# Optimization experiments

Hardware: AMD Instinct MI355X
Metric: run time of the kernel (lower is better)

## Reference

```python
import jax, jax.numpy as jnp
import numpy as np

T, B, I, H, L = 2048, 64, 256, 256, 2


def setup_inputs() -> dict:
    key = jax.random.key(0)
    ks = jax.random.split(key, 11)
    s = 1.0 / np.sqrt(H)  # torch LSTMCell reset_parameters: U(-1/sqrt(H), 1/sqrt(H))
    u = lambda k, shape: jax.random.uniform(k, shape, jnp.float32, -s, s)
    return {
        "input_": jax.random.normal(ks[0], (T, B, I), jnp.float32),
        "mask": (jax.random.uniform(ks[1], (T, B)) < 0.95).astype(jnp.float32),
        "reset_indices": (jax.random.uniform(ks[2], (T, B)) < 0.02).astype(jnp.float32),
        "W_ih0": u(ks[3], (4 * H, I)),
        "W_hh0": u(ks[4], (4 * H, H)),
        "b_ih0": u(ks[5], (4 * H,)),
        "b_hh0": u(ks[6], (4 * H,)),
        "W_ih1": u(ks[7], (4 * H, H)),
        "W_hh1": u(ks[8], (4 * H, H)),
        "b_ih1": u(ks[9], (4 * H,)),
        "b_hh1": u(ks[10], (4 * H,)),
    }


def _run_layer(x, mask, reset, W_ih, W_hh, b_ih, b_hh):
    # Precompute input projection for all timesteps as one big GEMM: [T,B,4H]
    xg = jnp.einsum('tbi,gi->tbg', x, W_ih) + b_ih + b_hh
    Bx = x.shape[1]
    Hh = W_hh.shape[1]

    def step(carry, xs):
        h, c = carry
        g_x, m_t, r_t = xs
        gates = g_x + h @ W_hh.T  # [B,4H]
        i, f, g, o = jnp.split(gates, 4, axis=-1)
        c_new = jax.nn.sigmoid(f) * c + jax.nn.sigmoid(i) * jnp.tanh(g)
        h_new = jax.nn.sigmoid(o) * jnp.tanh(c_new)
        m = m_t[:, None]
        h_b = h_new * m + h * (1.0 - m)   # mask blend (variable length)
        c_b = c_new * m + c * (1.0 - m)
        r = r_t[:, None]
        return (h_b * (1.0 - r), c_b * (1.0 - r)), h_b  # reset applied AFTER output

    h0 = jnp.zeros((Bx, Hh), x.dtype)
    (h_n, c_n), out = jax.lax.scan(step, (h0, h0), (xg, mask, reset))
    return out, h_n, c_n


def reference(input_, mask, reset_indices, W_ih0, W_hh0, b_ih0, b_hh0,
              W_ih1, W_hh1, b_ih1, b_hh1):
    # Faithful quirk of the original: every layer starts from the same zero hx.
    out0, h_n0, c_n0 = _run_layer(input_, mask, reset_indices, W_ih0, W_hh0, b_ih0, b_hh0)
    out1, h_n1, c_n1 = _run_layer(out0, mask, reset_indices, W_ih1, W_hh1, b_ih1, b_hh1)
    h_n = jnp.stack([h_n0, h_n1], 0)  # [L,B,H]
    c_n = jnp.stack([c_n0, c_n1], 0)
    return out1, h_n, c_n
```

## Files before the change

kernel.cpp:

```cpp
#include <hip/hip_runtime.h>
#include <cstdint>
#include <cstddef>

#define T_STEPS 2048
#define BB 64
#define II 256
#define HH 256
#define GG 1024
#define RING 64
#define VQ 23
#define LQ 9

static_assert((RING & (RING - 1)) == 0, "RING must be power of 2");
static_assert(VQ + LQ == 32, "full K coverage");

typedef _Float16 half2_t __attribute__((ext_vector_type(2)));
typedef unsigned u32x4_t __attribute__((ext_vector_type(4)));

static __device__ __forceinline__ float sigm(float x) {
    return 1.0f / (1.0f + __expf(-x));
}
static __device__ __forceinline__ float tanhfast(float x) {
    float e = __expf(2.0f * x);
    return 1.0f - 2.0f / (e + 1.0f);
}
static __device__ __forceinline__ float fd2(unsigned hu, unsigned wu, float acc) {
    union { unsigned u; half2_t v; } a, b;
    a.u = hu; b.u = wu;
    return __builtin_amdgcn_fdot2(a.v, b.v, acc, false);
}

static __device__ __forceinline__ unsigned aloadu(const unsigned* p) {
    return __hip_atomic_load((unsigned*)p, __ATOMIC_RELAXED, __HIP_MEMORY_SCOPE_AGENT);
}
static __device__ __forceinline__ void astoreu(unsigned* p, unsigned v) {
    __hip_atomic_store(p, v, __ATOMIC_RELAXED, __HIP_MEMORY_SCOPE_AGENT);
}
static __device__ __forceinline__ int aloadi(const int* p) {
    return __hip_atomic_load((int*)p, __ATOMIC_RELAXED, __HIP_MEMORY_SCOPE_AGENT);
}
static __device__ __forceinline__ void astorei(int* p, int v) {
    __hip_atomic_store(p, v, __ATOMIC_RELAXED, __HIP_MEMORY_SCOPE_AGENT);
}
#define CFENCE asm volatile("" ::: "memory")

__global__ void k_pack_w(const float* __restrict__ W, unsigned* __restrict__ wt) {
    int p = blockIdx.x;
    int row = threadIdx.x;
    float2 v = *(const float2*)(W + (size_t)row * HH + 2 * p);
    union { unsigned u; half2_t h; } cv;
    cv.h = half2_t{ (_Float16)v.x, (_Float16)v.y };
    wt[((size_t)(p >> 2) * 1024 + row) * 4 + (p & 3)] = cv.u;
}

__global__ void k_bias_sum(const float* __restrict__ a, const float* __restrict__ b,
                           float* __restrict__ o) {
    int i = threadIdx.x;
    o[i] = a[i] + b[i];
}

__global__ void k_init_prog(int* __restrict__ p) {
    p[threadIdx.x] = 0;
}

__global__ __launch_bounds__(256, 1)
__attribute__((amdgpu_waves_per_eu(1, 1)))
void k_pipe(const float* __restrict__ x,
            const float* __restrict__ mask,
            const float* __restrict__ reset,
            const u32x4_t* __restrict__ wih0,
            const u32x4_t* __restrict__ whh0,
            const u32x4_t* __restrict__ wih1,
            const u32x4_t* __restrict__ whh1,
            const float* __restrict__ bsum0,
            const float* __restrict__ bsum1,
            unsigned* __restrict__ gx0,
            unsigned* __restrict__ gx1,
            unsigned* __restrict__ h0r,
            float* __restrict__ out,
            float* __restrict__ hn,
            float* __restrict__ cn,
            int* __restrict__ prog)
{
    __shared__ __align__(16) u32x4_t wsh[LQ * 1024];
    __shared__ __align__(16) _Float16 hbuf[2][HH];

    const int stage = blockIdx.x >> 6;
    const int b = blockIdx.x & 63;
    const int tid = threadIdx.x;
    const int r0 = tid, r1 = tid + 256, r2 = tid + 512, r3 = tid + 768;

    const u32x4_t* w4 = (stage == 0) ? wih0 : (stage == 1) ? whh0
                      : (stage == 2) ? wih1 : whh1;

#pragma unroll
    for (int j = 0; j < LQ; ++j) {
        wsh[j * 1024 + r0] = w4[(size_t)(VQ + j) * 1024 + r0];
        wsh[j * 1024 + r1] = w4[(size_t)(VQ + j) * 1024 + r1];
        wsh[j * 1024 + r2] = w4[(size_t)(VQ + j) * 1024 + r2];
        wsh[j * 1024 + r3] = w4[(size_t)(VQ + j) * 1024 + r3];
    }
    unsigned wr0[4 * VQ], wr1[4 * VQ], wr2[4 * VQ], wr3[4 * VQ];
#pragma unroll
    for (int j = 0; j < VQ; ++j) {
        u32x4_t q;
        q = w4[(size_t)j * 1024 + r0]; wr0[4*j] = q.x; wr0[4*j+1] = q.y; wr0[4*j+2] = q.z; wr0[4*j+3] = q.w;
        q = w4[(size_t)j * 1024 + r1]; wr1[4*j] = q.x; wr1[4*j+1] = q.y; wr1[4*j+2] = q.z; wr1[4*j+3] = q.w;
        q = w4[(size_t)j * 1024 + r2]; wr2[4*j] = q.x; wr2[4*j+1] = q.y; wr2[4*j+2] = q.z; wr2[4*j+3] = q.w;
        q = w4[(size_t)j * 1024 + r3]; wr3[4*j] = q.x; wr3[4*j+1] = q.y; wr3[4*j+2] = q.z; wr3[4*j+3] = q.w;
    }
#pragma unroll
    for (int j = 0; j < 4 * VQ; ++j) {
        asm volatile("" : "+v"(wr0[j]));
        asm volatile("" : "+v"(wr1[j]));
        asm volatile("" : "+v"(wr2[j]));
        asm volatile("" : "+v"(wr3[j]));
    }

    float bs0 = 0.f, bs1 = 0.f, bs2 = 0.f, bs3 = 0.f;
    if (stage == 0 || stage == 2) {
        const float* bs = (stage == 0) ? bsum0 : bsum1;
        bs0 = bs[r0]; bs1 = bs[r1]; bs2 = bs[r2]; bs3 = bs[r3];
    }
    float hp = 0.f, cp = 0.f;

    hbuf[0][tid] = (stage == 0) ? (_Float16)x[(size_t)b * II + tid] : (_Float16)0.f;
    hbuf[1][tid] = (_Float16)0.f;

    int seen = 0, bp = 0;
    int* myf = prog + stage * BB + b;
    const int* srcf = prog + (stage > 0 ? stage - 1 : 0) * BB + b;
    const int* consf = prog + (stage < 3 ? stage + 1 : 3) * BB + b;
    __syncthreads();

    for (int t = 0; t < T_STEPS; ++t) {
        float xn = 0.f, mc = 0.f, rc = 0.f;
        unsigned gA = 0, gB = 0;

        if (stage == 0) {
            if (t + 1 < T_STEPS)
                xn = x[((size_t)(t + 1) * BB + b) * II + tid];
            if (t - bp > RING - 8) {
                bp = aloadi(consf);
                while (t - bp > RING - 8) { __builtin_amdgcn_s_sleep(8); bp = aloadi(consf); }
                CFENCE;
            }
        } else if (stage == 2) {
            if (seen <= t) {
                seen = aloadi(srcf);
                while (seen <= t) { __builtin_amdgcn_s_sleep(2); seen = aloadi(srcf); }
                CFENCE;
            }
            unsigned hu = aloadu(h0r + ((size_t)(t & (RING - 1)) * BB + b) * HH + tid);
            __syncthreads();
            if (tid == 0) { astorei(myf, t); CFENCE; }
            hbuf[0][tid] = (_Float16)__uint_as_float(hu);
            if (t - bp > RING - 8) {
                bp = aloadi(consf);
                while (t - bp > RING - 8) { __builtin_amdgcn_s_sleep(8); bp = aloadi(consf); }
                CFENCE;
            }
            __syncthreads();
        } else {
            if (seen <= t) {
                seen = aloadi(srcf);
                while (seen <= t) { __builtin_amdgcn_s_sleep(2); seen = aloadi(srcf); }
                CFENCE;
            }
            const unsigned* gring = (stage == 1) ? gx0 : gx1;
            size_t gbase = ((size_t)(t & (RING - 1)) * BB + b) * 512;
            gA = aloadu(gring + gbase + tid);
            gB = aloadu(gring + gbase + 256 + tid);
            mc = mask[(size_t)t * BB + b];
            rc = reset[(size_t)t * BB + b];
            if (stage == 1 && t - bp > RING - 8) {
                bp = aloadi(consf);
                while (t - bp > RING - 8) { __builtin_amdgcn_s_sleep(8); bp = aloadi(consf); }
                CFENCE;
            }
        }

        const u32x4_t* hsh = (const u32x4_t*)((stage == 2) ? hbuf[0] : hbuf[t & 1]);
        float a00 = 0.f, a01 = 0.f, a02 = 0.f, a03 = 0.f;
        float a10 = 0.f, a11 = 0.f, a12 = 0.f, a13 = 0.f;
        float a20 = 0.f, a21 = 0.f, a22 = 0.f, a23 = 0.f;
        float a30 = 0.f, a31 = 0.f, a32 = 0.f, a33 = 0.f;
#pragma unroll
        for (int j = 0; j < VQ; ++j) {
            u32x4_t hv = hsh[j];
            a00 = fd2(hv.x, wr0[4*j+0], a00); a01 = fd2(hv.y, wr0[4*j+1], a01);
            a02 = fd2(hv.z, wr0[4*j+2], a02); a03 = fd2(hv.w, wr0[4*j+3], a03);
            a10 = fd2(hv.x, wr1[4*j+0], a10); a11 = fd2(hv.y, wr1[4*j+1], a11);
            a12 = fd2(hv.z, wr1[4*j+2], a12); a13 = fd2(hv.w, wr1[4*j+3], a13);
            a20 = fd2(hv.x, wr2[4*j+0], a20); a21 = fd2(hv.y, wr2[4*j+1], a21);
            a22 = fd2(hv.z, wr2[4*j+2], a22); a23 = fd2(hv.w, wr2[4*j+3], a23);
            a30 = fd2(hv.x, wr3[4*j+0], a30); a31 = fd2(hv.y, wr3[4*j+1], a31);
            a32 = fd2(hv.z, wr3[4*j+2], a32); a33 = fd2(hv.w, wr3[4*j+3], a33);
        }
#pragma unroll
        for (int j = 0; j < LQ; ++j) {
            u32x4_t hv = hsh[VQ + j];
            u32x4_t w0 = wsh[j * 1024 + r0];
            a00 = fd2(hv.x, w0.x, a00); a01 = fd2(hv.y, w0.y, a01);
            a02 = fd2(hv.z, w0.z, a02); a03 = fd2(hv.w, w0.w, a03);
            u32x4_t w1 = wsh[j * 1024 + r1];
            a10 = fd2(hv.x, w1.x, a10); a11 = fd2(hv.y, w1.y, a11);
            a12 = fd2(hv.z, w1.z, a12); a13 = fd2(hv.w, w1.w, a13);
            u32x4_t w2 = wsh[j * 1024 + r2];
            a20 = fd2(hv.x, w2.x, a20); a21 = fd2(hv.y, w2.y, a21);
            a22 = fd2(hv.z, w2.z, a22); a23 = fd2(hv.w, w2.w, a23);
            u32x4_t w3 = wsh[j * 1024 + r3];
            a30 = fd2(hv.x, w3.x, a30); a31 = fd2(hv.y, w3.y, a31);
            a32 = fd2(hv.z, w3.z, a32); a33 = fd2(hv.w, w3.w, a33);
        }
        float s0 = (a00 + a01) + (a02 + a03);
        float s1 = (a10 + a11) + (a12 + a13);
        float s2 = (a20 + a21) + (a22 + a23);
        float s3 = (a30 + a31) + (a32 + a33);

        if (stage == 0 || stage == 2) {
            s0 += bs0; s1 += bs1; s2 += bs2; s3 += bs3;
            unsigned* gring = (stage == 0) ? gx0 : gx1;
            size_t gbase = ((size_t)(t & (RING - 1)) * BB + b) * 512;
            union { unsigned u; half2_t h; } pa, pb;
            pa.h = half2_t{ (_Float16)s0, (_Float16)s2 };
            pb.h = half2_t{ (_Float16)s1, (_Float16)s3 };
            astoreu(gring + gbase + tid, pa.u);
            astoreu(gring + gbase + 256 + tid, pb.u);
            if (stage == 0) {
                hbuf[(t + 1) & 1][tid] = (_Float16)xn;
                __syncthreads();
                if (tid == 0) { astorei(myf, t + 1); CFENCE; }
            }
        } else {
            union { unsigned u; half2_t h; } ua, ub;
            ua.u = gA; ub.u = gB;
            float si = s0 + (float)ua.h.x;
            float sf = s1 + (float)ub.h.x;
            float sg = s2 + (float)ua.h.y;
            float so = s3 + (float)ub.h.y;
            float i_ = sigm(si), f_ = sigm(sf), g_ = tanhfast(sg), o_ = sigm(so);
            float cnew = f_ * cp + i_ * g_;
            float hnew = o_ * tanhfast(cnew);
            float hb = hnew * mc + hp * (1.f - mc);
            float cb = cnew * mc + cp * (1.f - mc);
            if (stage == 1)
                astoreu(h0r + ((size_t)(t & (RING - 1)) * BB + b) * HH + tid,
                        __float_as_uint(hb));
            else
                out[(size_t)t * (BB * HH) + (size_t)b * HH + tid] = hb;
            hp = hb * (1.f - rc);
            cp = cb * (1.f - rc);
            hbuf[(t + 1) & 1][tid] = (_Float16)hp;
            __syncthreads();
            if (tid == 0) { astorei(myf, t + 1); CFENCE; }
        }
    }

    if (stage == 2) {
        __syncthreads();
        if (tid == 0) { astorei(myf, T_STEPS); CFENCE; }
    }
    if (stage == 1 || stage == 3) {
        int L = (stage == 3);
        hn[((size_t)L * BB + b) * HH + tid] = hp;
        cn[((size_t)L * BB + b) * HH + tid] = cp;
    }
}

extern "C" void kernel_launch(void* const* d_in, const int* in_sizes, int n_in,
                              void* d_out, int out_size, void* d_ws, size_t ws_size,
                              hipStream_t stream) {
    (void)in_sizes; (void)n_in; (void)out_size; (void)ws_size;
    const float* input = (const float*)d_in[0];
    const float* maskp = (const float*)d_in[1];
    const float* resetp = (const float*)d_in[2];
    const float* Wih0 = (const float*)d_in[3];
    const float* Whh0 = (const float*)d_in[4];
    const float* bih0 = (const float*)d_in[5];
    const float* bhh0 = (const float*)d_in[6];
    const float* Wih1 = (const float*)d_in[7];
    const float* Whh1 = (const float*)d_in[8];
    const float* bih1 = (const float*)d_in[9];
    const float* bhh1 = (const float*)d_in[10];

    const size_t WPACK = (size_t)GG * HH * 2;
    char* p = (char*)d_ws;
    unsigned* wih0t = (unsigned*)p; p += WPACK;
    unsigned* whh0t = (unsigned*)p; p += WPACK;
    unsigned* wih1t = (unsigned*)p; p += WPACK;
    unsigned* whh1t = (unsigned*)p; p += WPACK;
    float* bsum0 = (float*)p; p += GG * sizeof(float);
    float* bsum1 = (float*)p; p += GG * sizeof(float);
    int* prog = (int*)p; p += 4096;
    unsigned* gx0 = (unsigned*)p; p += (size_t)RING * BB * 512 * 4;
    unsigned* gx1 = (unsigned*)p; p += (size_t)RING * BB * 512 * 4;
    unsigned* h0r = (unsigned*)p; p += (size_t)RING * BB * 256 * 4;

    float* out1 = (float*)d_out;
    float* hn = out1 + (size_t)T_STEPS * BB * HH;
    float* cn = hn + 2 * (size_t)BB * HH;

    k_pack_w<<<dim3(HH / 2), 1024, 0, stream>>>(Wih0, wih0t);
    k_pack_w<<<dim3(HH / 2), 1024, 0, stream>>>(Whh0, whh0t);
    k_pack_w<<<dim3(HH / 2), 1024, 0, stream>>>(Wih1, wih1t);
    k_pack_w<<<dim3(HH / 2), 1024, 0, stream>>>(Whh1, whh1t);
    k_bias_sum<<<dim3(1), GG, 0, stream>>>(bih0, bhh0, bsum0);
    k_bias_sum<<<dim3(1), GG, 0, stream>>>(bih1, bhh1, bsum1);
    k_init_prog<<<dim3(1), 256, 0, stream>>>(prog);

    const float* a_x = input; const float* a_m = maskp; const float* a_r = resetp;
    const u32x4_t* a_w0 = (const u32x4_t*)wih0t;
    const u32x4_t* a_w1 = (const u32x4_t*)whh0t;
    const u32x4_t* a_w2 = (const u32x4_t*)wih1t;
    const u32x4_t* a_w3 = (const u32x4_t*)whh1t;
    const float* a_b0 = bsum0; const float* a_b1 = bsum1;
    unsigned* a_g0 = gx0; unsigned* a_g1 = gx1; unsigned* a_h0 = h0r;
    float* a_out = out1; float* a_hn = hn; float* a_cn = cn; int* a_pr = prog;
    void* args[] = { &a_x, &a_m, &a_r, &a_w0, &a_w1, &a_w2, &a_w3, &a_b0, &a_b1,
                     &a_g0, &a_g1, &a_h0, &a_out, &a_hn, &a_cn, &a_pr };

    hipError_t err = hipLaunchCooperativeKernel((const void*)k_pipe, dim3(4 * BB),
                                                dim3(256), args, 0, stream);
    if (err != hipSuccess) {
        (void)hipGetLastError();
        k_pipe<<<dim3(4 * BB), dim3(256), 0, stream>>>(
            a_x, a_m, a_r, a_w0, a_w1, a_w2, a_w3, a_b0, a_b1,
            a_g0, a_g1, a_h0, a_out, a_hn, a_cn, a_pr);
    }
}
```

Measured before the change: 8.268 ms.

## Rewrite LSTM pipeline as hidden-slice MFMA kernel with per-layer slice sync

Replaces the 256-block, per-batch, four-stage fdot2 pipeline with 32 blocks (16 hidden slices per layer). Each block holds its fp16 weight slices in registers and computes input and recurrent projections for all 64 batch rows with 16x16x32 MFMA instructions. Blocks exchange fp16 hidden state through global ring buffers, with a wave-wide spin on slice progress flags. The input is converted to fp16 up front. The aim is to use the matrix cores and cut per-step sync and launch width, at the cost of all-to-all slice synchronisation every step and extra fp16 rounding of the input.

```diff
diff --git a/kernel.cpp b/kernel.cpp
--- a/kernel.cpp
+++ b/kernel.cpp
@@ -8,14 +8,12 @@
 #define HH 256
 #define GG 1024
 #define RING 64
-#define VQ 23
-#define LQ 9
-
-static_assert((RING & (RING - 1)) == 0, "RING must be power of 2");
-static_assert(VQ + LQ == 32, "full K coverage");
-
-typedef _Float16 half2_t __attribute__((ext_vector_type(2)));
-typedef unsigned u32x4_t __attribute__((ext_vector_type(4)));
+#define NSL 16
+#define DPS 16
+
+typedef _Float16 half8_t __attribute__((ext_vector_type(8)));
+typedef float    f32x4_t __attribute__((ext_vector_type(4)));
+typedef unsigned long long u64;
 
 static __device__ __forceinline__ float sigm(float x) {
     return 1.0f / (1.0f + __expf(-x));
@@ -24,16 +22,11 @@
     float e = __expf(2.0f * x);
     return 1.0f - 2.0f / (e + 1.0f);
 }
-static __device__ __forceinline__ float fd2(unsigned hu, unsigned wu, float acc) {
-    union { unsigned u; half2_t v; } a, b;
-    a.u = hu; b.u = wu;
-    return __builtin_amdgcn_fdot2(a.v, b.v, acc, false);
-}
-
-static __device__ __forceinline__ unsigned aloadu(const unsigned* p) {
-    return __hip_atomic_load((unsigned*)p, __ATOMIC_RELAXED, __HIP_MEMORY_SCOPE_AGENT);
-}
-static __device__ __forceinline__ void astoreu(unsigned* p, unsigned v) {
+
+static __device__ __forceinline__ u64 aload64(const u64* p) {
+    return __hip_atomic_load((u64*)p, __ATOMIC_RELAXED, __HIP_MEMORY_SCOPE_AGENT);
+}
+static __device__ __forceinline__ void astore64(u64* p, u64 v) {
     __hip_atomic_store(p, v, __ATOMIC_RELAXED, __HIP_MEMORY_SCOPE_AGENT);
 }
 static __device__ __forceinline__ int aloadi(const int* p) {
@@ -44,13 +37,16 @@
 }
 #define CFENCE asm volatile("" ::: "memory")
 
-__global__ void k_pack_w(const float* __restrict__ W, unsigned* __restrict__ wt) {
-    int p = blockIdx.x;
-    int row = threadIdx.x;
-    float2 v = *(const float2*)(W + (size_t)row * HH + 2 * p);
-    union { unsigned u; half2_t h; } cv;
-    cv.h = half2_t{ (_Float16)v.x, (_Float16)v.y };
-    wt[((size_t)(p >> 2) * 1024 + row) * 4 + (p & 3)] = cv.u;
+union H8 { struct { u64 lo, hi; } u; half8_t v; };
+
+__global__ void k_f32_to_f16(const float* __restrict__ in, _Float16* __restrict__ out, int n) {
+    int i = (blockIdx.x * blockDim.x + threadIdx.x) * 4;
+    if (i >= n) return;
+    float4 v = *(const float4*)(in + i);
+    half8_t h;
+    h[0] = (_Float16)v.x; h[1] = (_Float16)v.y; h[2] = (_Float16)v.z; h[3] = (_Float16)v.w;
+    *(_Float16*)(out + i) = h[0];
+    out[i + 1] = h[1]; out[i + 2] = h[2]; out[i + 3] = h[3];
 }
 
 __global__ void k_bias_sum(const float* __restrict__ a, const float* __restrict__ b,
@@ -59,212 +55,213 @@
     o[i] = a[i] + b[i];
 }
 
-__global__ void k_init_prog(int* __restrict__ p) {
-    p[threadIdx.x] = 0;
+__global__ void k_init(_Float16* __restrict__ hR, int* __restrict__ prog) {
+    int L = blockIdx.x >> 3, part = blockIdx.x & 7;
+    size_t off = ((size_t)L * RING + (RING - 1)) * (BB * HH) + (size_t)part * 2048
+               + (size_t)threadIdx.x * 8;
+    ((u64*)(hR + off))[0] = 0ull;
+    ((u64*)(hR + off))[1] = 0ull;
+    if (blockIdx.x == 0 && threadIdx.x < 64) prog[threadIdx.x] = 0;
 }
 
 __global__ __launch_bounds__(256, 1)
 __attribute__((amdgpu_waves_per_eu(1, 1)))
-void k_pipe(const float* __restrict__ x,
+void k_pipe(const _Float16* __restrict__ xh,
+            const _Float16* __restrict__ w0ih,
+            const _Float16* __restrict__ w0hh,
+            const _Float16* __restrict__ w1ih,
+            const _Float16* __restrict__ w1hh,
+            const float* __restrict__ bsum0,
+            const float* __restrict__ bsum1,
             const float* __restrict__ mask,
             const float* __restrict__ reset,
-            const u32x4_t* __restrict__ wih0,
-            const u32x4_t* __restrict__ whh0,
-            const u32x4_t* __restrict__ wih1,
-            const u32x4_t* __restrict__ whh1,
-            const float* __restrict__ bsum0,
-            const float* __restrict__ bsum1,
-            unsigned* __restrict__ gx0,
-            unsigned* __restrict__ gx1,
-            unsigned* __restrict__ h0r,
+            _Float16* __restrict__ hR,
+            _Float16* __restrict__ hX,
             float* __restrict__ out,
             float* __restrict__ hn,
             float* __restrict__ cn,
             int* __restrict__ prog)
 {
-    __shared__ __align__(16) u32x4_t wsh[LQ * 1024];
-    __shared__ __align__(16) _Float16 hbuf[2][HH];
-
-    const int stage = blockIdx.x >> 6;
-    const int b = blockIdx.x & 63;
+    __shared__ __align__(16) float acts[4 * DPS * BB];
+    __shared__ __align__(16) _Float16 hsR[BB * DPS];
+    __shared__ __align__(16) _Float16 hsX[BB * DPS];
+    __shared__ __align__(16) float osF[BB * DPS];
+
+    const int L   = blockIdx.x >> 4;
+    const int sl  = blockIdx.x & 15;
     const int tid = threadIdx.x;
-    const int r0 = tid, r1 = tid + 256, r2 = tid + 512, r3 = tid + 768;
-
-    const u32x4_t* w4 = (stage == 0) ? wih0 : (stage == 1) ? whh0
-                      : (stage == 2) ? wih1 : whh1;
-
-#pragma unroll
-    for (int j = 0; j < LQ; ++j) {
-        wsh[j * 1024 + r0] = w4[(size_t)(VQ + j) * 1024 + r0];
-        wsh[j * 1024 + r1] = w4[(size_t)(VQ + j) * 1024 + r1];
-        wsh[j * 1024 + r2] = w4[(size_t)(VQ + j) * 1024 + r2];
-        wsh[j * 1024 + r3] = w4[(size_t)(VQ + j) * 1024 + r3];
+    const int lane = tid & 63, l15 = lane & 15, q = lane >> 4;
+    const int wave = tid >> 6;
+    const int waveN = wave & 1;
+    const int waveM = wave >> 1;
+
+    const _Float16* Wih = L ? w1ih : w0ih;
+    const _Float16* Whh = L ? w1hh : w0hh;
+    const float* bsum = L ? bsum1 : bsum0;
+
+    const int grow0 = waveN * 256 + sl * DPS + l15;
+    const int grow1 = (waveN + 2) * 256 + sl * DPS + l15;
+    half8_t bih[2][8], bhh[2][8];
+#pragma unroll
+    for (int kj = 0; kj < 8; ++kj) {
+        bih[0][kj] = *(const half8_t*)(Wih + (size_t)grow0 * HH + kj * 32 + q * 8);
+        bih[1][kj] = *(const half8_t*)(Wih + (size_t)grow1 * HH + kj * 32 + q * 8);
+        bhh[0][kj] = *(const half8_t*)(Whh + (size_t)grow0 * HH + kj * 32 + q * 8);
+        bhh[1][kj] = *(const half8_t*)(Whh + (size_t)grow1 * HH + kj * 32 + q * 8);
     }
-    unsigned wr0[4 * VQ], wr1[4 * VQ], wr2[4 * VQ], wr3[4 * VQ];
-#pragma unroll
-    for (int j = 0; j < VQ; ++j) {
-        u32x4_t q;
-        q = w4[(size_t)j * 1024 + r0]; wr0[4*j] = q.x; wr0[4*j+1] = q.y; wr0[4*j+2] = q.z; wr0[4*j+3] = q.w;
-        q = w4[(size_t)j * 1024 + r1]; wr1[4*j] = q.x; wr1[4*j+1] = q.y; wr1[4*j+2] = q.z; wr1[4*j+3] = q.w;
-        q = w4[(size_t)j * 1024 + r2]; wr2[4*j] = q.x; wr2[4*j+1] = q.y; wr2[4*j+2] = q.z; wr2[4*j+3] = q.w;
-        q = w4[(size_t)j * 1024 + r3]; wr3[4*j] = q.x; wr3[4*j+1] = q.y; wr3[4*j+2] = q.z; wr3[4*j+3] = q.w;
+    const float bsv0 = bsum[grow0], bsv1 = bsum[grow1];
+
+    const int jf = tid & 15, bf = (tid >> 4) * 4;
+    float cS[4] = {0.f, 0.f, 0.f, 0.f};
+    float hS[4] = {0.f, 0.f, 0.f, 0.f};
+
+    const int rowA0 = (2 * waveM + 0) * 16 + l15;
+    const int rowA1 = (2 * waveM + 1) * 16 + l15;
+
+    int* myf = prog + L * NSL + sl;
+
+    for (int t = 0; t < T_STEPS; ++t) {
+        if (wave == 0) {
+            const int* fp = nullptr; int tgt = -2147483647;
+            if (lane < 16) { fp = prog + L * NSL + lane; tgt = t; }
+            else if (lane < 32) {
+                fp = L ? (prog + (lane - 16)) : (prog + NSL + (lane - 16));
+                tgt = L ? (t + 1) : (t - (RING - 4));
+            }
+            int v = 0x7fffffff;
+            if (fp) v = aloadi(fp);
+            while (!__all(v >= tgt)) {
+                __builtin_amdgcn_s_sleep(1);
+                if (fp) v = aloadi(fp);
+            }
+            CFENCE;
+        }
+        __syncthreads();
+
+        H8 hA[2][8];
+        const _Float16* hsrc = hR + ((size_t)L * RING + ((t + RING - 1) & (RING - 1))) * (BB * HH);
+#pragma unroll
+        for (int kj = 0; kj < 8; ++kj) {
+            const u64* p0 = (const u64*)(hsrc + (size_t)rowA0 * HH + kj * 32 + q * 8);
+            const u64* p1 = (const u64*)(hsrc + (size_t)rowA1 * HH + kj * 32 + q * 8);
+            hA[0][kj].u.lo = aload64(p0); hA[0][kj].u.hi = aload64(p0 + 1);
+            hA[1][kj].u.lo = aload64(p1); hA[1][kj].u.hi = aload64(p1 + 1);
+        }
+
+        half8_t xa[2][8];
+        if (L == 0) {
+            const _Float16* xs = xh + (size_t)t * (BB * HH);
+#pragma unroll
+            for (int kj = 0; kj < 8; ++kj) {
+                xa[0][kj] = *(const half8_t*)(xs + (size_t)rowA0 * HH + kj * 32 + q * 8);
+                xa[1][kj] = *(const half8_t*)(xs + (size_t)rowA1 * HH + kj * 32 + q * 8);
+            }
+        } else {
+            const _Float16* xs = hX + (size_t)(t & (RING - 1)) * (BB * HH);
+#pragma unroll
+            for (int kj = 0; kj < 8; ++kj) {
+                H8 a, b;
+                const u64* p0 = (const u64*)(xs + (size_t)rowA0 * HH + kj * 32 + q * 8);
+                const u64* p1 = (const u64*)(xs + (size_t)rowA1 * HH + kj * 32 + q * 8);
+                a.u.lo = aload64(p0); a.u.hi = aload64(p0 + 1);
+                b.u.lo = aload64(p1); b.u.hi = aload64(p1 + 1);
+                xa[0][kj] = a.v; xa[1][kj] = b.v;
+            }
+        }
+
+        const float4 mv = *(const float4*)(mask + (size_t)t * BB + bf);
+        const float4 rv = *(const float4*)(reset + (size_t)t * BB + bf);
+
+        f32x4_t acc[2][2];
+        acc[0][0] = f32x4_t{bsv0, bsv0, bsv0, bsv0};
+        acc[0][1] = f32x4_t{bsv1, bsv1, bsv1, bsv1};
+        acc[1][0] = f32x4_t{bsv0, bsv0, bsv0, bsv0};
+        acc[1][1] = f32x4_t{bsv1, bsv1, bsv1, bsv1};
+#pragma unroll
+        for (int kj = 0; kj < 8; ++kj) {
+            acc[0][0] = __builtin_amdgcn_mfma_f32_16x16x32_f16(xa[0][kj], bih[0][kj], acc[0][0], 0, 0, 0);
+            acc[0][1] = __builtin_amdgcn_mfma_f32_16x16x32_f16(xa[0][kj], bih[1][kj], acc[0][1], 0, 0, 0);
+            acc[1][0] = __builtin_amdgcn_mfma_f32_16x16x32_f16(xa[1][kj], bih[0][kj], acc[1][0], 0, 0, 0);
+            acc[1][1] = __builtin_amdgcn_mfma_f32_16x16x32_f16(xa[1][kj], bih[1][kj], acc[1][1], 0, 0, 0);
+        }
+#pragma unroll
+        for (int kj = 0; kj < 8; ++kj) {
+            acc[0][0] = __builtin_amdgcn_mfma_f32_16x16x32_f16(hA[0][kj].v, bhh[0][kj], acc[0][0], 0, 0, 0);
+            acc[0][1] = __builtin_amdgcn_mfma_f32_16x16x32_f16(hA[0][kj].v, bhh[1][kj], acc[0][1], 0, 0, 0);
+            acc[1][0] = __builtin_amdgcn_mfma_f32_16x16x32_f16(hA[1][kj].v, bhh[0][kj], acc[1][0], 0, 0, 0);
+            acc[1][1] = __builtin_amdgcn_mfma_f32_16x16x32_f16(hA[1][kj].v, bhh[1][kj], acc[1][1], 0, 0, 0);
+        }
+
+#pragma unroll
+        for (int mm = 0; mm < 2; ++mm) {
+#pragma unroll
+            for (int p = 0; p < 2; ++p) {
+                const int g = waveN + 2 * p;
+                f32x4_t av;
+#pragma unroll
+                for (int r = 0; r < 4; ++r) {
+                    float s = acc[mm][p][r];
+                    av[r] = (g == 2) ? tanhfast(s) : sigm(s);
+                }
+                unsigned dwoff = (unsigned)(((g * DPS + l15) * BB) + (2 * waveM + mm) * 16 + q * 4);
+                unsigned byteoff = (dwoff * 4u) ^ ((unsigned)(l15 & 7) << 4);
+                *(f32x4_t*)((char*)acts + byteoff) = av;
+            }
+        }
+        __syncthreads();
+
+        {
+            f32x4_t gi, gf_, gg, go;
+            {
+                unsigned swz = ((unsigned)(jf & 7) << 4);
+                gi  = *(const f32x4_t*)((const char*)acts + ((((0 * DPS + jf) * BB + bf) * 4u) ^ swz));
+                gf_ = *(const f32x4_t*)((const char*)acts + ((((1 * DPS + jf) * BB + bf) * 4u) ^ swz));
+                gg  = *(const f32x4_t*)((const char*)acts + ((((2 * DPS + jf) * BB + bf) * 4u) ^ swz));
+                go  = *(const f32x4_t*)((const char*)acts + ((((3 * DPS + jf) * BB + bf) * 4u) ^ swz));
+            }
+            const float mm4[4] = {mv.x, mv.y, mv.z, mv.w};
+            const float rr4[4] = {rv.x, rv.y, rv.z, rv.w};
+#pragma unroll
+            for (int e = 0; e < 4; ++e) {
+                float cnew = gf_[e] * cS[e] + gi[e] * gg[e];
+                float hnew = go[e] * tanhfast(cnew);
+                float m = mm4[e], r = rr4[e];
+                float hb = hnew * m + hS[e] * (1.f - m);
+                float cb = cnew * m + cS[e] * (1.f - m);
+                hS[e] = hb * (1.f - r);
+                cS[e] = cb * (1.f - r);
+                hsR[(bf + e) * DPS + jf] = (_Float16)hS[e];
+                if (L == 0) hsX[(bf + e) * DPS + jf] = (_Float16)hb;
+                else        osF[(bf + e) * DPS + jf] = hb;
+            }
+        }
+        __syncthreads();
+
+        {
+            const int b = tid >> 2, joff = (tid & 3) * 4;
+            u64 vR = *(const u64*)(hsR + b * DPS + joff);
+            _Float16* dR = hR + ((size_t)L * RING + (t & (RING - 1))) * (BB * HH)
+                         + (size_t)b * HH + sl * DPS + joff;
+            astore64((u64*)dR, vR);
+            if (L == 0) {
+                u64 vX = *(const u64*)(hsX + b * DPS + joff);
+                _Float16* dX = hX + (size_t)(t & (RING - 1)) * (BB * HH)
+                             + (size_t)b * HH + sl * DPS + joff;
+                astore64((u64*)dX, vX);
+            } else {
+                const int bo = tid >> 2;
+                f32x4_t ov = *(const f32x4_t*)(osF + bo * DPS + joff);
+                *(f32x4_t*)(out + ((size_t)t * BB + bo) * HH + sl * DPS + joff) = ov;
+            }
+        }
+        __syncthreads();
+        if (tid == 0) { astorei(myf, t + 1); CFENCE; }
     }
-#pragma unroll
-    for (int j = 0; j < 4 * VQ; ++j) {
-        asm volatile("" : "+v"(wr0[j]));
-        asm volatile("" : "+v"(wr1[j]));
-        asm volatile("" : "+v"(wr2[j]));
-        asm volatile("" : "+v"(wr3[j]));
-    }
-
-    float bs0 = 0.f, bs1 = 0.f, bs2 = 0.f, bs3 = 0.f;
-    if (stage == 0 || stage == 2) {
-        const float* bs = (stage == 0) ? bsum0 : bsum1;
-        bs0 = bs[r0]; bs1 = bs[r1]; bs2 = bs[r2]; bs3 = bs[r3];
-    }
-    float hp = 0.f, cp = 0.f;
-
-    hbuf[0][tid] = (stage == 0) ? (_Float16)x[(size_t)b * II + tid] : (_Float16)0.f;
-    hbuf[1][tid] = (_Float16)0.f;
-
-    int seen = 0, bp = 0;
-    int* myf = prog + stage * BB + b;
-    const int* srcf = prog + (stage > 0 ? stage - 1 : 0) * BB + b;
-    const int* consf = prog + (stage < 3 ? stage + 1 : 3) * BB + b;
-    __syncthreads();
-
-    for (int t = 0; t < T_STEPS; ++t) {
-        float xn = 0.f, mc = 0.f, rc = 0.f;
-        unsigned gA = 0, gB = 0;
-
-        if (stage == 0) {
-            if (t + 1 < T_STEPS)
-                xn = x[((size_t)(t + 1) * BB + b) * II + tid];
-            if (t - bp > RING - 8) {
-                bp = aloadi(consf);
-                while (t - bp > RING - 8) { __builtin_amdgcn_s_sleep(8); bp = aloadi(consf); }
-                CFENCE;
-            }
-        } else if (stage == 2) {
-            if (seen <= t) {
-                seen = aloadi(srcf);
-                while (seen <= t) { __builtin_amdgcn_s_sleep(2); seen = aloadi(srcf); }
-                CFENCE;
-            }
-            unsigned hu = aloadu(h0r + ((size_t)(t & (RING - 1)) * BB + b) * HH + tid);
-            __syncthreads();
-            if (tid == 0) { astorei(myf, t); CFENCE; }
-            hbuf[0][tid] = (_Float16)__uint_as_float(hu);
-            if (t - bp > RING - 8) {
-                bp = aloadi(consf);
-                while (t - bp > RING - 8) { __builtin_amdgcn_s_sleep(8); bp = aloadi(consf); }
-                CFENCE;
-            }
-            __syncthreads();
-        } else {
-            if (seen <= t) {
-                seen = aloadi(srcf);
-                while (seen <= t) { __builtin_amdgcn_s_sleep(2); seen = aloadi(srcf); }
-                CFENCE;
-            }
-            const unsigned* gring = (stage == 1) ? gx0 : gx1;
-            size_t gbase = ((size_t)(t & (RING - 1)) * BB + b) * 512;
-            gA = aloadu(gring + gbase + tid);
-            gB = aloadu(gring + gbase + 256 + tid);
-            mc = mask[(size_t)t * BB + b];
-            rc = reset[(size_t)t * BB + b];
-            if (stage == 1 && t - bp > RING - 8) {
-                bp = aloadi(consf);
-                while (t - bp > RING - 8) { __builtin_amdgcn_s_sleep(8); bp = aloadi(consf); }
-                CFENCE;
-            }
-        }
-
-        const u32x4_t* hsh = (const u32x4_t*)((stage == 2) ? hbuf[0] : hbuf[t & 1]);
-        float a00 = 0.f, a01 = 0.f, a02 = 0.f, a03 = 0.f;
-        float a10 = 0.f, a11 = 0.f, a12 = 0.f, a13 = 0.f;
-        float a20 = 0.f, a21 = 0.f, a22 = 0.f, a23 = 0.f;
-        float a30 = 0.f, a31 = 0.f, a32 = 0.f, a33 = 0.f;
-#pragma unroll
-        for (int j = 0; j < VQ; ++j) {
-            u32x4_t hv = hsh[j];
-            a00 = fd2(hv.x, wr0[4*j+0], a00); a01 = fd2(hv.y, wr0[4*j+1], a01);
-            a02 = fd2(hv.z, wr0[4*j+2], a02); a03 = fd2(hv.w, wr0[4*j+3], a03);
-            a10 = fd2(hv.x, wr1[4*j+0], a10); a11 = fd2(hv.y, wr1[4*j+1], a11);
-            a12 = fd2(hv.z, wr1[4*j+2], a12); a13 = fd2(hv.w, wr1[4*j+3], a13);
-            a20 = fd2(hv.x, wr2[4*j+0], a20); a21 = fd2(hv.y, wr2[4*j+1], a21);
-            a22 = fd2(hv.z, wr2[4*j+2], a22); a23 = fd2(hv.w, wr2[4*j+3], a23);
-            a30 = fd2(hv.x, wr3[4*j+0], a30); a31 = fd2(hv.y, wr3[4*j+1], a31);
-            a32 = fd2(hv.z, wr3[4*j+2], a32); a33 = fd2(hv.w, wr3[4*j+3], a33);
-        }
-#pragma unroll
-        for (int j = 0; j < LQ; ++j) {
-            u32x4_t hv = hsh[VQ + j];
-            u32x4_t w0 = wsh[j * 1024 + r0];
-            a00 = fd2(hv.x, w0.x, a00); a01 = fd2(hv.y, w0.y, a01);
-            a02 = fd2(hv.z, w0.z, a02); a03 = fd2(hv.w, w0.w, a03);
-            u32x4_t w1 = wsh[j * 1024 + r1];
-            a10 = fd2(hv.x, w1.x, a10); a11 = fd2(hv.y, w1.y, a11);
-            a12 = fd2(hv.z, w1.z, a12); a13 = fd2(hv.w, w1.w, a13);
-            u32x4_t w2 = wsh[j * 1024 + r2];
-            a20 = fd2(hv.x, w2.x, a20); a21 = fd2(hv.y, w2.y, a21);
-            a22 = fd2(hv.z, w2.z, a22); a23 = fd2(hv.w, w2.w, a23);
-            u32x4_t w3 = wsh[j * 1024 + r3];
-            a30 = fd2(hv.x, w3.x, a30); a31 = fd2(hv.y, w3.y, a31);
-            a32 = fd2(hv.z, w3.z, a32); a33 = fd2(hv.w, w3.w, a33);
-        }
-        float s0 = (a00 + a01) + (a02 + a03);
-        float s1 = (a10 + a11) + (a12 + a13);
-        float s2 = (a20 + a21) + (a22 + a23);
-        float s3 = (a30 + a31) + (a32 + a33);
-
-        if (stage == 0 || stage == 2) {
-            s0 += bs0; s1 += bs1; s2 += bs2; s3 += bs3;
-            unsigned* gring = (stage == 0) ? gx0 : gx1;
-            size_t gbase = ((size_t)(t & (RING - 1)) * BB + b) * 512;
-            union { unsigned u; half2_t h; } pa, pb;
-            pa.h = half2_t{ (_Float16)s0, (_Float16)s2 };
-            pb.h = half2_t{ (_Float16)s1, (_Float16)s3 };
-            astoreu(gring + gbase + tid, pa.u);
-            astoreu(gring + gbase + 256 + tid, pb.u);
-            if (stage == 0) {
-                hbuf[(t + 1) & 1][tid] = (_Float16)xn;
-                __syncthreads();
-                if (tid == 0) { astorei(myf, t + 1); CFENCE; }
-            }
-        } else {
-            union { unsigned u; half2_t h; } ua, ub;
-            ua.u = gA; ub.u = gB;
-            float si = s0 + (float)ua.h.x;
-            float sf = s1 + (float)ub.h.x;
-            float sg = s2 + (float)ua.h.y;
-            float so = s3 + (float)ub.h.y;
-            float i_ = sigm(si), f_ = sigm(sf), g_ = tanhfast(sg), o_ = sigm(so);
-            float cnew = f_ * cp + i_ * g_;
-            float hnew = o_ * tanhfast(cnew);
-            float hb = hnew * mc + hp * (1.f - mc);
-            float cb = cnew * mc + cp * (1.f - mc);
-            if (stage == 1)
-                astoreu(h0r + ((size_t)(t & (RING - 1)) * BB + b) * HH + tid,
-                        __float_as_uint(hb));
-            else
-                out[(size_t)t * (BB * HH) + (size_t)b * HH + tid] = hb;
-            hp = hb * (1.f - rc);
-            cp = cb * (1.f - rc);
-            hbuf[(t + 1) & 1][tid] = (_Float16)hp;
-            __syncthreads();
-            if (tid == 0) { astorei(myf, t + 1); CFENCE; }
-        }
-    }
-
-    if (stage == 2) {
-        __syncthreads();
-        if (tid == 0) { astorei(myf, T_STEPS); CFENCE; }
-    }
-    if (stage == 1 || stage == 3) {
-        int L = (stage == 3);
-        hn[((size_t)L * BB + b) * HH + tid] = hp;
-        cn[((size_t)L * BB + b) * HH + tid] = cp;
+
+#pragma unroll
+    for (int e = 0; e < 4; ++e) {
+        hn[((size_t)L * BB + bf + e) * HH + sl * DPS + jf] = hS[e];
+        cn[((size_t)L * BB + bf + e) * HH + sl * DPS + jf] = cS[e];
     }
 }
 
@@ -284,48 +281,47 @@
     const float* bih1 = (const float*)d_in[9];
     const float* bhh1 = (const float*)d_in[10];
 
-    const size_t WPACK = (size_t)GG * HH * 2;
     char* p = (char*)d_ws;
-    unsigned* wih0t = (unsigned*)p; p += WPACK;
-    unsigned* whh0t = (unsigned*)p; p += WPACK;
-    unsigned* wih1t = (unsigned*)p; p += WPACK;
-    unsigned* whh1t = (unsigned*)p; p += WPACK;
-    float* bsum0 = (float*)p; p += GG * sizeof(float);
-    float* bsum1 = (float*)p; p += GG * sizeof(float);
-    int* prog = (int*)p; p += 4096;
-    unsigned* gx0 = (unsigned*)p; p += (size_t)RING * BB * 512 * 4;
-    unsigned* gx1 = (unsigned*)p; p += (size_t)RING * BB * 512 * 4;
-    unsigned* h0r = (unsigned*)p; p += (size_t)RING * BB * 256 * 4;
+    _Float16* xh = (_Float16*)p;    p += (size_t)T_STEPS * BB * II * 2;
+    _Float16* w0ihh = (_Float16*)p; p += (size_t)GG * II * 2;
+    _Float16* w0hhh = (_Float16*)p; p += (size_t)GG * HH * 2;
+    _Float16* w1ihh = (_Float16*)p; p += (size_t)GG * HH * 2;
+    _Float16* w1hhh = (_Float16*)p; p += (size_t)GG * HH * 2;
+    float* bsum0 = (float*)p;       p += GG * sizeof(float);
+    float* bsum1 = (float*)p;       p += GG * sizeof(float);
+    _Float16* hRr = (_Float16*)p;   p += (size_t)2 * RING * BB * HH * 2;
+    _Float16* hXr = (_Float16*)p;   p += (size_t)RING * BB * HH * 2;
+    int* prog = (int*)p;            p += 4096;
 
     float* out1 = (float*)d_out;
     float* hn = out1 + (size_t)T_STEPS * BB * HH;
     float* cn = hn + 2 * (size_t)BB * HH;
 
-    k_pack_w<<<dim3(HH / 2), 1024, 0, stream>>>(Wih0, wih0t);
-    k_pack_w<<<dim3(HH / 2), 1024, 0, stream>>>(Whh0, whh0t);
-    k_pack_w<<<dim3(HH / 2), 1024, 0, stream>>>(Wih1, wih1t);
-    k_pack_w<<<dim3(HH / 2), 1024, 0, stream>>>(Whh1, whh1t);
+    k_f32_to_f16<<<dim3((T_STEPS * BB * II) / 1024), 256, 0, stream>>>(input, xh, T_STEPS * BB * II);
+    k_f32_to_f16<<<dim3((GG * II) / 1024), 256, 0, stream>>>(Wih0, w0ihh, GG * II);
+    k_f32_to_f16<<<dim3((GG * HH) / 1024), 256, 0, stream>>>(Whh0, w0hhh, GG * HH);
+    k_f32_to_f16<<<dim3((GG * HH) / 1024), 256, 0, stream>>>(Wih1, w1ihh, GG * HH);
+    k_f32_to_f16<<<dim3((GG * HH) / 1024), 256, 0, stream>>>(Whh1, w1hhh, GG * HH);
     k_bias_sum<<<dim3(1), GG, 0, stream>>>(bih0, bhh0, bsum0);
     k_bias_sum<<<dim3(1), GG, 0, stream>>>(bih1, bhh1, bsum1);
-    k_init_prog<<<dim3(1), 256, 0, stream>>>(prog);
-
-    const float* a_x = input; const float* a_m = maskp; const float* a_r = resetp;
-    const u32x4_t* a_w0 = (const u32x4_t*)wih0t;
-    const u32x4_t* a_w1 = (const u32x4_t*)whh0t;
-    const u32x4_t* a_w2 = (const u32x4_t*)wih1t;
-    const u32x4_t* a_w3 = (const u32x4_t*)whh1t;
+    k_init<<<dim3(16), 256, 0, stream>>>(hRr, prog);
+
+    const _Float16* a_xh = xh;
+    const _Float16* a_w0i = w0ihh; const _Float16* a_w0h = w0hhh;
+    const _Float16* a_w1i = w1ihh; const _Float16* a_w1h = w1hhh;
     const float* a_b0 = bsum0; const float* a_b1 = bsum1;
-    unsigned* a_g0 = gx0; unsigned* a_g1 = gx1; unsigned* a_h0 = h0r;
+    const float* a_m = maskp; const float* a_r = resetp;
+    _Float16* a_hR = hRr; _Float16* a_hX = hXr;
     float* a_out = out1; float* a_hn = hn; float* a_cn = cn; int* a_pr = prog;
-    void* args[] = { &a_x, &a_m, &a_r, &a_w0, &a_w1, &a_w2, &a_w3, &a_b0, &a_b1,
-                     &a_g0, &a_g1, &a_h0, &a_out, &a_hn, &a_cn, &a_pr };
-
-    hipError_t err = hipLaunchCooperativeKernel((const void*)k_pipe, dim3(4 * BB),
+    void* args[] = { &a_xh, &a_w0i, &a_w0h, &a_w1i, &a_w1h, &a_b0, &a_b1,
+                     &a_m, &a_r, &a_hR, &a_hX, &a_out, &a_hn, &a_cn, &a_pr };
+
+    hipError_t err = hipLaunchCooperativeKernel((const void*)k_pipe, dim3(2 * NSL),
                                                 dim3(256), args, 0, stream);
     if (err != hipSuccess) {
         (void)hipGetLastError();
-        k_pipe<<<dim3(4 * BB), dim3(256), 0, stream>>>(
-            a_x, a_m, a_r, a_w0, a_w1, a_w2, a_w3, a_b0, a_b1,
-            a_g0, a_g1, a_h0, a_out, a_hn, a_cn, a_pr);
+        k_pipe<<<dim3(2 * NSL), dim3(256), 0, stream>>>(
+            a_xh, a_w0i, a_w0h, a_w1i, a_w1h, a_b0, a_b1,
+            a_m, a_r, a_hR, a_hX, a_out, a_hn, a_cn, a_pr);
     }
 }
```

Result: slower. 21.69 ms (+162.3%).
